# Kernel optimization log

Hardware: AMD Instinct MI355X
Metric: run time of the kernel (lower is better)

Reference implementation:

```python
import jax, jax.numpy as jnp
import numpy as np

NUM_BEAMS = 2


def setup_inputs() -> dict:
    key = jax.random.key(0)
    ks = jax.random.split(key, 5)
    B, T, H, E, F = 128, 32, 768, 4, 3072
    x = jax.random.normal(ks[0], (B, T, H), dtype=jnp.float32)
    Wg = jax.random.normal(ks[1], (E, H), dtype=jnp.float32) * (1.0 / np.sqrt(H))
    W1 = jax.random.normal(ks[2], (E, H, F), dtype=jnp.float32) * (1.0 / np.sqrt(H))
    b1 = jnp.zeros((E, F), dtype=jnp.float32)
    W2 = jax.random.normal(ks[3], (E, F, H), dtype=jnp.float32) * (1.0 / np.sqrt(F))
    b2 = jnp.zeros((E, H), dtype=jnp.float32)
    return {"x": x, "Wg": Wg, "W1": W1, "b1": b1, "W2": W2, "b2": b2}


def reference(x, Wg, W1, b1, W2, b2):
    B, T, H = x.shape
    E = Wg.shape[0]
    nb = NUM_BEAMS
    # ---- forward_gate: mask is all-ones, so masked mean == mean over tokens ----
    x_avg = jnp.mean(x, axis=1)                          # [B, H]
    logits_gate = x_avg @ Wg.T                           # [B, E]
    prob_gate = jax.nn.softmax(logits_gate, axis=-1)     # [B, E]
    # ---- importance auxiliary loss (torch.std uses ddof=1) ----
    importance = jnp.sum(prob_gate, axis=0)              # [E]
    importance_loss = (jnp.std(importance, ddof=1) / jnp.mean(importance)) ** 2
    # ---- beam search, first layer: exp(log(p)) == p, top-k per row ----
    current_scores = jnp.exp(jnp.log(prob_gate))         # == prob_gate (kept for fidelity)
    topk_values, gate_idx = jax.lax.top_k(current_scores, nb)   # [B, nb]
    beam_scores = topk_values.reshape(nb * B)            # row-major flatten, matches .view
    expert_route = gate_idx.reshape(nb * B)[:, None]     # [B*nb, 1]
    beam_idx = jnp.arange(nb * B)
    current_expert_select = expert_route[:, -1]          # [B*nb]
    # ---- first layer: replicate x and scores along beam dim (interleaved) ----
    x_rep = jnp.repeat(x, nb, axis=0)                    # [B*nb, T, H]
    scores_rep = jnp.repeat(prob_gate, nb, axis=0)       # [B*nb, E]
    # input_x = x_rep[beam_idx] is identity here (beam_idx == arange)
    # ---- forward_expert_ffn: run ALL experts, mask+combine with gate prob ----
    h1 = jnp.einsum('bth,ehf->betf', x_rep, W1) + b1[None, :, None, :]
    h1 = jax.nn.gelu(h1, approximate=False)              # torch GELU is exact erf form
    cand = jnp.einsum('betf,efh->beth', h1, W2) + b2[None, :, None, :]  # [B*nb, E, T, H]
    weight = scores_rep * jax.nn.one_hot(current_expert_select, E, dtype=scores_rep.dtype)
    output = jnp.einsum('beth,be->bth', cand, weight)    # weighted sum over experts
    return output, beam_scores, expert_route, beam_idx, importance_loss
```

## Files before the change

kernel.cpp:

```cpp
#include <hip/hip_runtime.h>
#include <math.h>

typedef _Float16 f16;
typedef _Float16 f16x8 __attribute__((ext_vector_type(8)));
typedef float f32x4 __attribute__((ext_vector_type(4)));

#define Bn 128
#define Tn 32
#define Hn 768
#define En 4
#define Fn 3072
#define Rn 256

static constexpr size_t OUT_ELEMS  = (size_t)Rn*Tn*Hn;
static constexpr size_t SCORES_OFF = OUT_ELEMS;
static constexpr size_t ROUTE_OFF  = OUT_ELEMS + Rn;
static constexpr size_t BIDX_OFF   = OUT_ELEMS + 2*Rn;
static constexpr size_t LOSS_OFF   = OUT_ELEMS + 3*Rn;

#define WS_WSF    0u
#define WS_ROUTE  4096u
#define WS_GRP    8192u
#define WS_X16    16384u
#define WS_W1T    (WS_X16 + 2u*Bn*Tn*Hn)
#define WS_W2T    (WS_W1T + 2u*En*Hn*Fn)
#define WS_H1     (WS_W2T + 2u*En*Fn*Hn)

#define GLOAD16(g, l) __builtin_amdgcn_global_load_lds( \
    (const __attribute__((address_space(1))) unsigned int*)(g), \
    (__attribute__((address_space(3))) unsigned int*)(l), 16, 0, 0)

__device__ __forceinline__ float fast_gelu(float v) {
  float s = v * 0.70710678118f;
  float a = fabsf(s);
  float t = 1.0f / (1.0f + 0.3275911f * a);
  float y = t*(0.254829592f + t*(-0.284496736f + t*(1.421413741f +
            t*(-1.453152027f + t*1.061405429f))));
  float er = 1.0f - y * __expf(-a*a);
  er = (s < 0.0f) ? -er : er;
  return 0.5f * v * (1.0f + er);
}

__global__ __launch_bounds__(64) void gate_kernel(
    const float* __restrict__ x, const float* __restrict__ Wg,
    float* __restrict__ out, float* __restrict__ wsf, int* __restrict__ route)
{
  const int b = blockIdx.x;
  const int l = threadIdx.x;
  float acc0=0.f, acc1=0.f, acc2=0.f, acc3=0.f;
  const float* xb = x + (size_t)b*Tn*Hn;
  for (int h = l; h < Hn; h += 64) {
    float xa = 0.f;
    #pragma unroll
    for (int t = 0; t < Tn; ++t) xa += xb[t*Hn + h];
    xa *= (1.0f/Tn);
    acc0 += xa * Wg[0*Hn + h];
    acc1 += xa * Wg[1*Hn + h];
    acc2 += xa * Wg[2*Hn + h];
    acc3 += xa * Wg[3*Hn + h];
  }
  #pragma unroll
  for (int o = 32; o > 0; o >>= 1) {
    acc0 += __shfl_down(acc0, o);
    acc1 += __shfl_down(acc1, o);
    acc2 += __shfl_down(acc2, o);
    acc3 += __shfl_down(acc3, o);
  }
  if (l == 0) {
    float lg[4] = {acc0, acc1, acc2, acc3};
    float m = fmaxf(fmaxf(lg[0],lg[1]), fmaxf(lg[2],lg[3]));
    float p[4]; float s = 0.f;
    #pragma unroll
    for (int e = 0; e < 4; ++e) { p[e] = expf(lg[e]-m); s += p[e]; }
    float inv = 1.f/s;
    #pragma unroll
    for (int e = 0; e < 4; ++e) { p[e] *= inv; wsf[b*4+e] = p[e]; }
    int i1 = 0;
    #pragma unroll
    for (int e = 1; e < 4; ++e) if (p[e] > p[i1]) i1 = e;
    int i2 = (i1 == 0) ? 1 : 0;
    #pragma unroll
    for (int e = 0; e < 4; ++e) if (e != i1 && p[e] > p[i2]) i2 = e;
    int idx[2] = {i1, i2};
    #pragma unroll
    for (int k = 0; k < 2; ++k) {
      int r = 2*b + k;
      float pv = p[idx[k]];
      wsf[512 + r] = pv;
      route[r] = idx[k];
      out[SCORES_OFF + r] = pv;
      out[ROUTE_OFF  + r] = (float)idx[k];
      out[BIDX_OFF   + r] = (float)r;
    }
  }
}

__global__ __launch_bounds__(64) void loss_kernel(
    const float* __restrict__ wsf, float* __restrict__ out)
{
  const int l = threadIdx.x;
  float i0=0.f,i1=0.f,i2=0.f,i3=0.f;
  for (int b = l; b < Bn; b += 64) {
    i0 += wsf[b*4+0]; i1 += wsf[b*4+1]; i2 += wsf[b*4+2]; i3 += wsf[b*4+3];
  }
  #pragma unroll
  for (int o = 32; o > 0; o >>= 1) {
    i0 += __shfl_down(i0,o); i1 += __shfl_down(i1,o);
    i2 += __shfl_down(i2,o); i3 += __shfl_down(i3,o);
  }
  if (l == 0) {
    float mean = 0.25f*(i0+i1+i2+i3);
    float d0=i0-mean, d1=i1-mean, d2=i2-mean, d3=i3-mean;
    float var = (d0*d0+d1*d1+d2*d2+d3*d3) * (1.f/3.f);
    out[LOSS_OFF] = var / (mean*mean);
  }
}

__global__ __launch_bounds__(64) void group_kernel(
    const int* __restrict__ route, int* __restrict__ grp)
{
  const int l = threadIdx.x;
  int cnt = 0;
  if (l < 4) { for (int r = 0; r < Rn; ++r) cnt += (route[r] == l); }
  int c0 = __shfl(cnt, 0), c1 = __shfl(cnt, 1), c2 = __shfl(cnt, 2), c3 = __shfl(cnt, 3);
  int off = (l >= 1 ? c0 : 0) + (l >= 2 ? c1 : 0) + (l >= 3 ? c2 : 0);
  if (l < 4) {
    int p = off;
    for (int r = 0; r < Rn; ++r) if (route[r] == l) grp[128 + p++] = r;
  }
  if (l == 0) {
    int cs[4] = {c0, c1, c2, c3};
    int os[4] = {0, c0, c0+c1, c0+c1+c2};
    int nt = 0;
    for (int e = 0; e < 4; ++e) {
      for (int s = 0; s < cs[e]; s += 8) {
        int nb = cs[e] - s; if (nb > 8) nb = 8;
        grp[8+nt*3+0] = e; grp[8+nt*3+1] = os[e]+s; grp[8+nt*3+2] = nb;
        ++nt;
      }
    }
    grp[0] = nt;
  }
}

__global__ __launch_bounds__(256) void convx_kernel(
    const float* __restrict__ x, f16* __restrict__ x16)
{
  const int i = (blockIdx.x*256 + threadIdx.x) * 8;
  float4 a = *(const float4*)(x + i);
  float4 b = *(const float4*)(x + i + 4);
  union { f16 h[8]; uint4 u; } p;
  p.h[0]=(f16)a.x; p.h[1]=(f16)a.y; p.h[2]=(f16)a.z; p.h[3]=(f16)a.w;
  p.h[4]=(f16)b.x; p.h[5]=(f16)b.y; p.h[6]=(f16)b.z; p.h[7]=(f16)b.w;
  *(uint4*)(x16 + i) = p.u;
}

__global__ __launch_bounds__(256) void transcvt_kernel(
    const float* __restrict__ src, f16* __restrict__ dst, int R, int C)
{
  __shared__ f16 t[64][74];
  const int e  = blockIdx.z;
  const int r0 = blockIdx.y*64, c0 = blockIdx.x*64;
  const float* s = src + (size_t)e*R*C;
  f16* d = dst + (size_t)e*R*C;
  const int tid = threadIdx.x;
  const int i  = tid >> 2;
  const int j0 = (tid & 3) * 16;
  #pragma unroll
  for (int q = 0; q < 16; q += 4) {
    float4 v = *(const float4*)(s + (size_t)(r0+i)*C + c0 + j0 + q);
    t[i][j0+q+0]=(f16)v.x; t[i][j0+q+1]=(f16)v.y; t[i][j0+q+2]=(f16)v.z; t[i][j0+q+3]=(f16)v.w;
  }
  __syncthreads();
  f16 o[16];
  #pragma unroll
  for (int q = 0; q < 16; ++q) o[q] = t[j0+q][i];
  *(uint4*)(d + (size_t)(c0+i)*R + r0 + j0)     = *(uint4*)&o[0];
  *(uint4*)(d + (size_t)(c0+i)*R + r0 + j0 + 8) = *(uint4*)&o[8];
}

template<int KD, int ND, int BN, int NI, bool G1>
__global__ __launch_bounds__(1024, 4) void gemm_kernel(
    const f16* __restrict__ A16, const f16* __restrict__ B16,
    const float* __restrict__ bias, f16* __restrict__ oh,
    float* __restrict__ of, const int* __restrict__ grp,
    const float* __restrict__ wsf)
{
  const int ntiles = grp[0];
  const int tix = blockIdx.x;
  if (tix >= ntiles) return;
  const int e      = grp[8+tix*3+0];
  const int bstart = grp[8+tix*3+1];
  const int nb     = grp[8+tix*3+2];
  const int n0     = blockIdx.y * BN;
  const int tid    = threadIdx.x;
  const int lane   = tid & 63;
  const int w      = tid >> 6;

  extern __shared__ __align__(16) char smem[];
  constexpr int BNB = BN * 128;
  constexpr int BI  = BN / 128;

  const int srow8 = lane >> 3;
  const int sunit = (lane & 7) ^ srow8;
  const f16* asrc[2];
  #pragma unroll
  for (int i = 0; i < 2; ++i) {
    int row = (w*2 + i)*8 + srow8;
    int slot = row >> 5; if (slot >= nb) slot = nb - 1;
    int beam = grp[128 + bstart + slot];
    size_t rbase = G1 ? ((size_t)(beam>>1)*Tn + (row&31)) * (size_t)KD
                      : ((size_t)beam*Tn + (row&31)) * (size_t)KD;
    asrc[i] = A16 + rbase + sunit*8;
  }
  const f16* bsrc[BI];
  #pragma unroll
  for (int i = 0; i < BI; ++i) {
    int row = (w*BI + i)*8 + srow8;
    bsrc[i] = B16 + (size_t)e*ND*KD + (size_t)(n0 + row)*KD + sunit*8;
  }

  const int wm = w >> 2, wn = w & 3;
  const int lr = lane & 15, lk = lane >> 4;
  const int rowA0 = wm*64;
  const int rowB0 = wn*(NI*16);
  const int r7 = lr & 7;
  const int u0 = (lk ^ r7) * 16;

  constexpr int MI = 4;
  f32x4 acc[MI][NI];
  #pragma unroll
  for (int i=0;i<MI;++i)
    #pragma unroll
    for (int j=0;j<NI;++j) acc[i][j] = (f32x4){0.f,0.f,0.f,0.f};

  constexpr int NT = KD/64;
  {
    char* Ad = smem + (w*2)*1024;
    GLOAD16(asrc[0], Ad);
    GLOAD16(asrc[1], Ad + 1024);
    char* Bd = smem + 65536 + (w*BI)*1024;
    #pragma unroll
    for (int i = 0; i < BI; ++i) GLOAD16(bsrc[i], Bd + i*1024);
  }
  __syncthreads();

  int buf = 0;
  for (int kt = 0; kt < NT; ++kt) {
    if (kt + 1 < NT) {
      const int nxt = buf ^ 1;
      char* Ad = smem + nxt*32768 + (w*2)*1024;
      GLOAD16(asrc[0] + (kt+1)*64, Ad);
      GLOAD16(asrc[1] + (kt+1)*64, Ad + 1024);
      char* Bd = smem + 65536 + nxt*BNB + (w*BI)*1024;
      #pragma unroll
      for (int i = 0; i < BI; ++i) GLOAD16(bsrc[i] + (kt+1)*64, Bd + i*1024);
    }
    const char* Ab = smem + buf*32768;
    const char* Bb = smem + 65536 + buf*BNB;
    #pragma unroll
    for (int ks = 0; ks < 2; ++ks) {
      const int ub = u0 ^ (ks << 6);
      f16x8 af[MI], bf[NI];
      #pragma unroll
      for (int mi=0;mi<MI;++mi)
        af[mi] = *(const f16x8*)(Ab + (rowA0 + mi*16 + lr)*128 + ub);
      #pragma unroll
      for (int ni=0;ni<NI;++ni)
        bf[ni] = *(const f16x8*)(Bb + (rowB0 + ni*16 + lr)*128 + ub);
      #pragma unroll
      for (int mi=0;mi<MI;++mi)
        #pragma unroll
        for (int ni=0;ni<NI;++ni)
          acc[mi][ni] = __builtin_amdgcn_mfma_f32_16x16x32_f16(af[mi], bf[ni], acc[mi][ni], 0, 0, 0);
    }
    __syncthreads();
    buf ^= 1;
  }

  const int nvalid = nb * Tn;
  char* cst = smem;

  if (G1) {
    float bvals[NI];
    #pragma unroll
    for (int ni=0;ni<NI;++ni) bvals[ni] = bias[e*ND + n0 + rowB0 + ni*16 + lr];
    #pragma unroll
    for (int mi=0;mi<MI;++mi){
      #pragma unroll
      for (int j=0;j<4;++j){
        const int m = rowA0 + mi*16 + (lane>>4)*4 + j;
        const int m7 = m & 7;
        #pragma unroll
        for (int ni=0;ni<NI;++ni){
          const int n = rowB0 + ni*16 + lr;
          float v = acc[mi][ni][j] + bvals[ni];
          f16 hv = (f16)fast_gelu(v);
          *(f16*)(cst + m*512 + (((n>>3)^m7)<<4) + (n&7)*2) = hv;
        }
      }
    }
  } else {
    #pragma unroll
    for (int mi=0;mi<MI;++mi){
      #pragma unroll
      for (int j=0;j<4;++j){
        const int m = rowA0 + mi*16 + (lane>>4)*4 + j;
        const int m7 = m & 7;
        #pragma unroll
        for (int ni=0;ni<NI;++ni){
          const int n = rowB0 + ni*16 + lr;
          *(float*)(cst + m*512 + (((n>>2)^m7)<<4) + (n&3)*4) = acc[mi][ni][j];
        }
      }
    }
  }
  __syncthreads();

  const int u  = tid & 31;
  const int tr = tid >> 5;
  if (G1) {
    #pragma unroll
    for (int it = 0; it < 8; ++it) {
      const int r = it*32 + tr;
      if (r >= nvalid) continue;
      const int beam = grp[128 + bstart + (r>>5)];
      uint4 v = *(const uint4*)(cst + r*512 + (((u&24)|((u&7)^(r&7)))<<4));
      *(uint4*)(oh + ((size_t)beam*Tn + (r&31))*(size_t)ND + n0 + u*8) = v;
    }
  } else {
    float4 b4 = *(const float4*)(bias + e*ND + n0 + u*4);
    #pragma unroll
    for (int it = 0; it < 8; ++it) {
      const int r = it*32 + tr;
      if (r >= nvalid) continue;
      const int beam = grp[128 + bstart + (r>>5)];
      const float sc = wsf[512 + beam];
      float4 v = *(const float4*)(cst + r*512 + (((u&24)|((u&7)^(r&7)))<<4));
      v.x = (v.x + b4.x)*sc; v.y = (v.y + b4.y)*sc;
      v.z = (v.z + b4.z)*sc; v.w = (v.w + b4.w)*sc;
      *(float4*)(of + ((size_t)beam*Tn + (r&31))*(size_t)Hn + n0 + u*4) = v;
    }
  }
}

extern "C" void kernel_launch(void* const* d_in, const int* in_sizes, int n_in,
                              void* d_out, int out_size, void* d_ws, size_t ws_size,
                              hipStream_t stream)
{
  const float* x  = (const float*)d_in[0];
  const float* Wg = (const float*)d_in[1];
  const float* W1 = (const float*)d_in[2];
  const float* b1 = (const float*)d_in[3];
  const float* W2 = (const float*)d_in[4];
  const float* b2 = (const float*)d_in[5];
  float* out = (float*)d_out;
  char* ws = (char*)d_ws;
  float* wsf  = (float*)(ws + WS_WSF);
  int*   route= (int*)(ws + WS_ROUTE);
  int*   grp  = (int*)(ws + WS_GRP);
  f16*   x16  = (f16*)(ws + WS_X16);
  f16*   w1t  = (f16*)(ws + WS_W1T);
  f16*   w2t  = (f16*)(ws + WS_W2T);
  f16*   h1   = (f16*)(ws + WS_H1);

  gate_kernel<<<Bn, 64, 0, stream>>>(x, Wg, out, wsf, route);
  group_kernel<<<1, 64, 0, stream>>>(route, grp);
  loss_kernel<<<1, 64, 0, stream>>>(wsf, out);
  convx_kernel<<<1536, 256, 0, stream>>>(x, x16);
  transcvt_kernel<<<dim3(48,12,4), 256, 0, stream>>>(W1, w1t, Hn, Fn);
  transcvt_kernel<<<dim3(12,48,4), 256, 0, stream>>>(W2, w2t, Fn, Hn);

  auto g1 = gemm_kernel<Hn, Fn, 256, 4, true>;
  auto g2 = gemm_kernel<Fn, Hn, 128, 2, false>;
  const int smB = 131072;
  hipFuncSetAttribute((const void*)g1, hipFuncAttributeMaxDynamicSharedMemorySize, smB);
  hipFuncSetAttribute((const void*)g2, hipFuncAttributeMaxDynamicSharedMemorySize, smB);
  g1<<<dim3(35,12), 1024, smB, stream>>>(x16, w1t, b1, h1, nullptr, grp, wsf);
  g2<<<dim3(35,6),  1024, smB, stream>>>(h1, w2t, b2, nullptr, out, grp, wsf);
}
```

Baseline: 207.4 us.

## Use explicit vmcnt waits, raw barriers and setprio in GEMM pipeline; flatten grid

Replaces __syncthreads in the double-buffered GEMM k-loop with an explicit s_waitcnt vmcnt that leaves the next stage's loads in flight, followed by raw s_barrier and sched_barrier fences. It raises wave priority around the MFMA block. The 2D grid is flattened to 1D so that the N-tiles of one group tile are launched consecutively, which may improve L2 reuse of A rows. The risk is a race if the vmcnt count does not match the number of outstanding direct-to-LDS loads.

```diff
diff --git a/kernel.cpp b/kernel.cpp
--- a/kernel.cpp
+++ b/kernel.cpp
@@ -186,13 +186,15 @@
     float* __restrict__ of, const int* __restrict__ grp,
     const float* __restrict__ wsf)
 {
+  constexpr int NY = ND / BN;
   const int ntiles = grp[0];
-  const int tix = blockIdx.x;
+  const int tix = blockIdx.x / NY;
+  const int ny  = blockIdx.x % NY;
   if (tix >= ntiles) return;
   const int e      = grp[8+tix*3+0];
   const int bstart = grp[8+tix*3+1];
   const int nb     = grp[8+tix*3+2];
-  const int n0     = blockIdx.y * BN;
+  const int n0     = ny * BN;
   const int tid    = threadIdx.x;
   const int lane   = tid & 63;
   const int w      = tid >> 6;
@@ -200,6 +202,7 @@
   extern __shared__ __align__(16) char smem[];
   constexpr int BNB = BN * 128;
   constexpr int BI  = BN / 128;
+  constexpr int NLD = 2 + BI;
 
   const int srow8 = lane >> 3;
   const int sunit = (lane & 7) ^ srow8;
@@ -235,27 +238,30 @@
     for (int j=0;j<NI;++j) acc[i][j] = (f32x4){0.f,0.f,0.f,0.f};
 
   constexpr int NT = KD/64;
-  {
-    char* Ad = smem + (w*2)*1024;
-    GLOAD16(asrc[0], Ad);
-    GLOAD16(asrc[1], Ad + 1024);
-    char* Bd = smem + 65536 + (w*BI)*1024;
-    #pragma unroll
-    for (int i = 0; i < BI; ++i) GLOAD16(bsrc[i], Bd + i*1024);
-  }
-  __syncthreads();
+
+  auto STAGE = [&](int bsel, int kt2) {
+    char* Ad = smem + bsel*32768 + (w*2)*1024;
+    GLOAD16(asrc[0] + kt2*64, Ad);
+    GLOAD16(asrc[1] + kt2*64, Ad + 1024);
+    char* Bd = smem + 65536 + bsel*BNB + (w*BI)*1024;
+    #pragma unroll
+    for (int i = 0; i < BI; ++i) GLOAD16(bsrc[i] + kt2*64, Bd + i*1024);
+  };
+
+  STAGE(0, 0);
 
   int buf = 0;
   for (int kt = 0; kt < NT; ++kt) {
     if (kt + 1 < NT) {
-      const int nxt = buf ^ 1;
-      char* Ad = smem + nxt*32768 + (w*2)*1024;
-      GLOAD16(asrc[0] + (kt+1)*64, Ad);
-      GLOAD16(asrc[1] + (kt+1)*64, Ad + 1024);
-      char* Bd = smem + 65536 + nxt*BNB + (w*BI)*1024;
-      #pragma unroll
-      for (int i = 0; i < BI; ++i) GLOAD16(bsrc[i] + (kt+1)*64, Bd + i*1024);
-    }
+      STAGE(buf ^ 1, kt + 1);
+      asm volatile("s_waitcnt vmcnt(%0)" :: "i"(NLD) : "memory");
+    } else {
+      asm volatile("s_waitcnt vmcnt(0)" ::: "memory");
+    }
+    __builtin_amdgcn_sched_barrier(0);
+    __builtin_amdgcn_s_barrier();
+    __builtin_amdgcn_sched_barrier(0);
+
     const char* Ab = smem + buf*32768;
     const char* Bb = smem + 65536 + buf*BNB;
     #pragma unroll
@@ -268,13 +274,16 @@
       #pragma unroll
       for (int ni=0;ni<NI;++ni)
         bf[ni] = *(const f16x8*)(Bb + (rowB0 + ni*16 + lr)*128 + ub);
+      __builtin_amdgcn_s_setprio(1);
       #pragma unroll
       for (int mi=0;mi<MI;++mi)
         #pragma unroll
         for (int ni=0;ni<NI;++ni)
           acc[mi][ni] = __builtin_amdgcn_mfma_f32_16x16x32_f16(af[mi], bf[ni], acc[mi][ni], 0, 0, 0);
-    }
-    __syncthreads();
+      __builtin_amdgcn_s_setprio(0);
+    }
+    __builtin_amdgcn_s_barrier();
+    __builtin_amdgcn_sched_barrier(0);
     buf ^= 1;
   }
 
@@ -376,6 +385,6 @@
   const int smB = 131072;
   hipFuncSetAttribute((const void*)g1, hipFuncAttributeMaxDynamicSharedMemorySize, smB);
   hipFuncSetAttribute((const void*)g2, hipFuncAttributeMaxDynamicSharedMemorySize, smB);
-  g1<<<dim3(35,12), 1024, smB, stream>>>(x16, w1t, b1, h1, nullptr, grp, wsf);
-  g2<<<dim3(35,6),  1024, smB, stream>>>(h1, w2t, b2, nullptr, out, grp, wsf);
-}
+  g1<<<35*12, 1024, smB, stream>>>(x16, w1t, b1, h1, nullptr, grp, wsf);
+  g2<<<35*6,  1024, smB, stream>>>(h1, w2t, b2, nullptr, out, grp, wsf);
+}
```

After: 200.0 us. 3.5% less time.
